# Kernel optimization log

Hardware: AMD Instinct MI355X
Metric: run time of the kernel (lower is better)

## Reference

```python
import jax, jax.numpy as jnp
import numpy as np

DIM = 384
B = 256
EPS = 1e-5


def _conv_replicate(x, W, pad):
    # x: [B,C,H,W], W: [O,I,kh,kw]; replicate (edge) padding then VALID conv
    x = jnp.pad(x, ((0, 0), (0, 0), (pad, pad), (pad, pad)), mode='edge')
    return jax.lax.conv_general_dilated(
        x, W, window_strides=(1, 1), padding='VALID',
        dimension_numbers=('NCHW', 'OIHW', 'NCHW'))


def _bn(x, g, b, m, v):
    scale = (g / jnp.sqrt(v + EPS))[None, :, None, None]
    return (x - m[None, :, None, None]) * scale + b[None, :, None, None]


def _clip_features(target, bbox):
    # target: [B, 576, C] -> vectorized per-sample crop + nearest resize to 12x12
    bb = bbox * 24.0
    x, y, w, h = bb[:, 0], bb[:, 1], bb[:, 2], bb[:, 3]
    l = (w + h) / 2
    l = jnp.sqrt((w + l) * (h + l))
    x_min = jnp.clip(jnp.ceil(x - l / 2), 0, 23).astype(jnp.int32)
    y_min = jnp.clip(jnp.ceil(y - l / 2), 0, 23).astype(jnp.int32)
    x_max = jnp.clip(jnp.trunc(x + l / 2), 0, 23).astype(jnp.int32)
    y_max = jnp.clip(jnp.trunc(y + l / 2), 0, 23).astype(jnp.int32)
    i12 = jnp.arange(12, dtype=jnp.int32)
    # nearest-neighbor source index: crop_start + floor(i * crop_size / 12)
    rows = y_min[:, None] + (i12[None, :] * (y_max - y_min)[:, None]) // 12  # [B,12]
    cols = x_min[:, None] + (i12[None, :] * (x_max - x_min)[:, None]) // 12  # [B,12]
    rows = jnp.clip(rows, 0, 23)
    cols = jnp.clip(cols, 0, 23)
    Bn, N, C = target.shape
    tflat = jnp.transpose(target, (0, 2, 1))  # [B, C, 576] (row-major 24x24)
    idx = rows[:, :, None] * 24 + cols[:, None, :]  # [B,12,12]
    idx = jnp.broadcast_to(idx.reshape(Bn, 1, 144), (Bn, C, 144))
    out = jnp.take_along_axis(tflat, idx, axis=2)  # [B, C, 144]
    return out.reshape(Bn, C, 12, 12)


def setup_inputs() -> dict:
    key = jax.random.key(0)
    ks = jax.random.split(key, 8)
    temp = jax.random.normal(ks[0], (B, 144, DIM), dtype=jnp.float32)
    target = jax.random.normal(ks[1], (B, 576, DIM), dtype=jnp.float32)
    u = jax.random.uniform(ks[2], (B, 4), dtype=jnp.float32)
    # centers in [0.3,0.7], sizes in [0.25,0.45] -> always a valid non-empty crop
    bbox = jnp.concatenate([0.3 + 0.4 * u[:, :2], 0.25 + 0.2 * u[:, 2:]], axis=1)
    W1 = jax.random.normal(ks[3], (DIM, DIM, 5, 5), dtype=jnp.float32) * 0.02
    W2 = jax.random.normal(ks[4], (DIM, DIM, 3, 3), dtype=jnp.float32) * 0.05
    g1 = jnp.ones((DIM,), jnp.float32)
    b1 = jnp.zeros((DIM,), jnp.float32)
    m1 = jax.random.normal(ks[5], (DIM,), dtype=jnp.float32) * 0.1
    v1 = jnp.ones((DIM,), jnp.float32)
    g2 = jnp.ones((DIM,), jnp.float32)
    b2 = jnp.zeros((DIM,), jnp.float32)
    m2 = jax.random.normal(ks[6], (DIM,), dtype=jnp.float32) * 0.1
    v2 = jnp.ones((DIM,), jnp.float32)
    return dict(temp=temp, target=target, bbox=bbox, W1=W1, g1=g1, b1=b1,
                m1=m1, v1=v1, W2=W2, g2=g2, b2=b2, m2=m2, v2=v2)


def reference(temp, target, bbox, W1, g1, b1, m1, v1, W2, g2, b2, m2, v2):
    ta = _clip_features(target, bbox)  # [B, C, 12, 12]
    h1 = jax.nn.leaky_relu(_bn(_conv_replicate(ta, W1, 2), g1, b1, m1, v1), 0.01)
    h2 = jax.nn.leaky_relu(_bn(_conv_replicate(h1, W2, 1), g2, b2, m2, v2), 0.01)
    Bn, N, C = temp.shape
    t = jnp.transpose(temp, (0, 2, 1)).reshape(Bn, C, 12, 12)
    out = (t + h2).reshape(Bn, C, 144)
    return jnp.transpose(out, (0, 2, 1))  # [B, 144, C]
```

## Files before the change

kernel.cpp:

```cpp
#include <hip/hip_runtime.h>
#include <math.h>

#define NBATCH 256
#define CDIM   384

typedef __attribute__((ext_vector_type(4))) float  f32x4;
typedef __attribute__((ext_vector_type(8))) __bf16 bf16x8;
typedef __attribute__((ext_vector_type(4))) __bf16 bf16x4;

__device__ __forceinline__ void load16(const void* g, void* l) {
    __builtin_amdgcn_global_load_lds(
        (const __attribute__((address_space(1))) void*)g,
        (__attribute__((address_space(3))) void*)l, 16, 0, 0);
}

__global__ __launch_bounds__(256) void gather_bf16(
    const float* __restrict__ target,
    const float* __restrict__ bbox,
    __bf16* __restrict__ ta)
{
    const int b = blockIdx.x, t = threadIdx.x;
    __shared__ int pos[144];

    if (t < 144) {
        const float bx0 = bbox[b * 4 + 0] * 24.f;
        const float by0 = bbox[b * 4 + 1] * 24.f;
        const float bw  = bbox[b * 4 + 2] * 24.f;
        const float bh  = bbox[b * 4 + 3] * 24.f;
        const float l0 = (bw + bh) * 0.5f;
        const float l  = sqrtf((bw + l0) * (bh + l0));
        const int xmin = (int)fminf(fmaxf(ceilf (bx0 - l * 0.5f), 0.f), 23.f);
        const int ymin = (int)fminf(fmaxf(ceilf (by0 - l * 0.5f), 0.f), 23.f);
        const int xmax = (int)fminf(fmaxf(truncf(bx0 + l * 0.5f), 0.f), 23.f);
        const int ymax = (int)fminf(fmaxf(truncf(by0 + l * 0.5f), 0.f), 23.f);
        const int i = t / 12, j = t % 12;
        int r = ymin + (i * (ymax - ymin)) / 12;
        int c = xmin + (j * (xmax - xmin)) / 12;
        r = min(max(r, 0), 23);
        c = min(max(c, 0), 23);
        pos[t] = r * 24 + c;
    }
    __syncthreads();

    const float* tb  = target + (size_t)b * 576 * 384;
    __bf16*      tab = ta     + (size_t)b * 144 * 384;
    for (int idx = t; idx < 144 * 96; idx += 256) {
        const int p = idx / 96, c4 = idx - p * 96;
        const float4 v = *(const float4*)&tb[(size_t)pos[p] * 384 + c4 * 4];
        bf16x4 o = { (__bf16)v.x, (__bf16)v.y, (__bf16)v.z, (__bf16)v.w };
        *(bf16x4*)&tab[(size_t)p * 384 + c4 * 4] = o;
    }
}

template <int TAPS>
__global__ __launch_bounds__(256) void prep_w(
    const float* __restrict__ W, __bf16* __restrict__ Wt)
{
    const int K = TAPS * 384;
    __shared__ float ws[TAPS * 384];
    const int oc = blockIdx.x;
    const float* src = W + (size_t)oc * K;
    for (int i = threadIdx.x; i < K; i += 256) ws[i] = src[i];
    __syncthreads();
    __bf16* dst = Wt + (size_t)oc * K;
    for (int i = threadIdx.x; i < K; i += 256) {
        const int tap = i / 384;
        const int ic  = i - tap * 384;
        dst[i] = (__bf16)ws[ic * TAPS + tap];
    }
}

template <int TAPS, int KW, int PAD, bool RESID>
__global__ __launch_bounds__(256, 3) void conv_mfma(
    const __bf16* __restrict__ A,
    const __bf16* __restrict__ Wt,
    const float* __restrict__ gg, const float* __restrict__ bb,
    const float* __restrict__ mm, const float* __restrict__ vv,
    const float* __restrict__ temp,
    void* __restrict__ outp)
{
    const int K  = TAPS * 384;
    const int IT = TAPS * 12;
    const int m0 = blockIdx.x * 128;
    const int n0 = blockIdx.y * 128;
    const int t  = threadIdx.x;
    const int lane  = t & 63, w = t >> 6;
    const int wm    = (w & 1) * 64, wn = (w >> 1) * 64;
    const int col16 = lane & 15,  quad = lane >> 4;

    __shared__ __bf16 As0[128 * 32], As1[128 * 32];
    __shared__ __bf16 Bs0[128 * 32], Bs1[128 * 32];

    const int r0   = t >> 2, slot = t & 3;
    const int kg   = slot ^ ((r0 >> 1) & 3);
    const int mrow0 = m0 + r0, mrow1 = m0 + r0 + 64;
    const int b0 = mrow0 / 144, p0 = mrow0 - b0 * 144;
    const int b1 = mrow1 / 144, p1 = mrow1 - b1 * 144;
    const int y0 = p0 / 12, x0 = p0 - y0 * 12;
    const int y1 = p1 / 12, x1 = p1 - y1 * 12;
    const __bf16* Ab0 = A + (size_t)b0 * 144 * 384 + kg * 8;
    const __bf16* Ab1 = A + (size_t)b1 * 144 * 384 + kg * 8;

    int offA[4], offB[4];
#pragma unroll
    for (int mi = 0; mi < 4; ++mi) {
        const int r = wm + mi * 16 + col16;
        offA[mi] = r * 32 + (quad ^ ((r >> 1) & 3)) * 8;
    }
#pragma unroll
    for (int ni = 0; ni < 4; ++ni) {
        const int r = wn + ni * 16 + col16;
        offB[ni] = r * 32 + (quad ^ ((r >> 1) & 3)) * 8;
    }

    f32x4 acc[4][4];
#pragma unroll
    for (int mi = 0; mi < 4; ++mi)
#pragma unroll
        for (int ni = 0; ni < 4; ++ni)
            acc[mi][ni] = (f32x4){0.f, 0.f, 0.f, 0.f};

    int jn = 0, tapn = 0;
    const __bf16* aT0;
    const __bf16* aT1;
    {
        const int sy0 = min(max(y0 - PAD, 0), 11), sx0 = min(max(x0 - PAD, 0), 11);
        const int sy1 = min(max(y1 - PAD, 0), 11), sx1 = min(max(x1 - PAD, 0), 11);
        aT0 = Ab0 + (size_t)(sy0 * 12 + sx0) * 384;
        aT1 = Ab1 + (size_t)(sy1 * 12 + sx1) * 384;
    }
    const __bf16* bT0 = Wt + (size_t)(n0 + r0)      * K + kg * 8;
    const __bf16* bT1 = Wt + (size_t)(n0 + r0 + 64) * K + kg * 8;

    auto issue = [&](__bf16* SA, __bf16* SB) {
        load16(aT0 + jn * 32, &SA[t * 8]);
        load16(aT1 + jn * 32, &SA[(t + 256) * 8]);
        load16(bT0 + jn * 32, &SB[t * 8]);
        load16(bT1 + jn * 32, &SB[(t + 256) * 8]);
    };
    auto advance = [&]() {
        if (++jn == 12) {
            jn = 0;
            ++tapn;
            if (tapn < TAPS) {
                const int ky = tapn / KW - PAD, kx = tapn % KW - PAD;
                const int sy0 = min(max(y0 + ky, 0), 11), sx0 = min(max(x0 + kx, 0), 11);
                const int sy1 = min(max(y1 + ky, 0), 11), sx1 = min(max(x1 + kx, 0), 11);
                aT0 = Ab0 + (size_t)(sy0 * 12 + sx0) * 384;
                aT1 = Ab1 + (size_t)(sy1 * 12 + sx1) * 384;
                bT0 += 384;
                bT1 += 384;
            }
        }
    };
    auto mfma_step = [&](const __bf16* SA, const __bf16* SB, bool do_issue,
                         __bf16* NA, __bf16* NB_) {
        __syncthreads();
        bf16x8 av[4], bv[4];
#pragma unroll
        for (int mi = 0; mi < 4; ++mi) av[mi] = *(const bf16x8*)&SA[offA[mi]];
#pragma unroll
        for (int ni = 0; ni < 4; ++ni) bv[ni] = *(const bf16x8*)&SB[offB[ni]];
        if (do_issue) issue(NA, NB_);
#pragma unroll
        for (int mi = 0; mi < 4; ++mi)
#pragma unroll
            for (int ni = 0; ni < 4; ++ni)
                acc[mi][ni] = __builtin_amdgcn_mfma_f32_16x16x32_bf16(
                    av[mi], bv[ni], acc[mi][ni], 0, 0, 0);
    };

    issue(As0, Bs0);

    for (int it2 = 0; it2 < IT; it2 += 2) {
        advance();
        mfma_step(As0, Bs0, true, As1, Bs1);
        advance();
        mfma_step(As1, Bs1, it2 + 2 < IT, As0, Bs0);
    }

#pragma unroll
    for (int ni = 0; ni < 4; ++ni) {
        const int gn = n0 + wn + ni * 16 + col16;
        const float scale = gg[gn] * rsqrtf(vv[gn] + 1e-5f);
        const float shift = bb[gn] - mm[gn] * scale;
        if (!RESID) {
            __bf16* h1 = (__bf16*)outp;
#pragma unroll
            for (int mi = 0; mi < 4; ++mi) {
                const int gm = m0 + wm + mi * 16 + quad * 4;
#pragma unroll
                for (int r = 0; r < 4; ++r) {
                    float v = acc[mi][ni][r] * scale + shift;
                    v = (v >= 0.f) ? v : 0.01f * v;
                    h1[(size_t)(gm + r) * 384 + gn] = (__bf16)v;
                }
            }
        } else {
            float* outF = (float*)outp;
#pragma unroll
            for (int mi = 0; mi < 4; ++mi) {
                const int gm = m0 + wm + mi * 16 + quad * 4;
#pragma unroll
                for (int r = 0; r < 4; ++r) {
                    float v = acc[mi][ni][r] * scale + shift;
                    v = (v >= 0.f) ? v : 0.01f * v;
                    outF[(size_t)(gm + r) * 384 + gn] =
                        temp[(size_t)(gm + r) * 384 + gn] + v;
                }
            }
        }
    }
}

extern "C" void kernel_launch(void* const* d_in, const int* in_sizes, int n_in,
                              void* d_out, int out_size, void* d_ws, size_t ws_size,
                              hipStream_t stream) {
    const float* temp   = (const float*)d_in[0];
    const float* target = (const float*)d_in[1];
    const float* bbox   = (const float*)d_in[2];
    const float* W1     = (const float*)d_in[3];
    const float* g1     = (const float*)d_in[4];
    const float* b1     = (const float*)d_in[5];
    const float* m1     = (const float*)d_in[6];
    const float* v1     = (const float*)d_in[7];
    const float* W2     = (const float*)d_in[8];
    const float* g2     = (const float*)d_in[9];
    const float* b2     = (const float*)d_in[10];
    const float* m2     = (const float*)d_in[11];
    const float* v2     = (const float*)d_in[12];
    float* out = (float*)d_out;

    __bf16* ta  = (__bf16*)d_ws;
    __bf16* h1  = ta  + (size_t)NBATCH * 144 * CDIM;
    __bf16* Wt1 = h1  + (size_t)NBATCH * 144 * CDIM;
    __bf16* Wt2 = Wt1 + (size_t)CDIM * 25 * CDIM;

    prep_w<25><<<dim3(CDIM), dim3(256), 0, stream>>>(W1, Wt1);
    prep_w<9><<<dim3(CDIM), dim3(256), 0, stream>>>(W2, Wt2);
    gather_bf16<<<dim3(NBATCH), dim3(256), 0, stream>>>(target, bbox, ta);

    conv_mfma<25, 5, 2, false><<<dim3(288, 3), dim3(256), 0, stream>>>(
        ta, Wt1, g1, b1, m1, v1, nullptr, (void*)h1);
    conv_mfma<9, 3, 1, true><<<dim3(288, 3), dim3(256), 0, stream>>>(
        h1, Wt2, g2, b2, m2, v2, temp, (void*)out);
}
```

Before: 901.9 us.

## Triple-buffer LDS tiles with explicit vmcnt waits in conv MFMA loop

Replaces the double-buffered K loop with a three-stage ring of LDS buffers, keeping two tile loads in flight. Each step waits with a manual s_waitcnt vmcnt(4) plus a raw s_barrier instead of __syncthreads, and raises wave priority around the MFMA block with s_setprio. The goal is to hide global-to-LDS load latency behind compute. In exchange LDS use grows from 32KB to 48KB per block, which may limit the requested 3 blocks per CU, and the hand-written wait counts must stay in step with the four loads issued per stage.

```diff
diff --git a/kernel.cpp b/kernel.cpp
--- a/kernel.cpp
+++ b/kernel.cpp
@@ -88,8 +88,8 @@
     const int wm    = (w & 1) * 64, wn = (w >> 1) * 64;
     const int col16 = lane & 15,  quad = lane >> 4;
 
-    __shared__ __bf16 As0[128 * 32], As1[128 * 32];
-    __shared__ __bf16 Bs0[128 * 32], Bs1[128 * 32];
+    __shared__ __bf16 As0[128 * 32], As1[128 * 32], As2[128 * 32];
+    __shared__ __bf16 Bs0[128 * 32], Bs1[128 * 32], Bs2[128 * 32];
 
     const int r0   = t >> 2, slot = t & 3;
     const int kg   = slot ^ ((r0 >> 1) & 3);
@@ -120,7 +120,7 @@
         for (int ni = 0; ni < 4; ++ni)
             acc[mi][ni] = (f32x4){0.f, 0.f, 0.f, 0.f};
 
-    int jn = 0, tapn = 0;
+    int jn = 0, tapn = 0, next = 0;
     const __bf16* aT0;
     const __bf16* aT1;
     {
@@ -153,30 +153,35 @@
             }
         }
     };
-    auto mfma_step = [&](const __bf16* SA, const __bf16* SB, bool do_issue,
-                         __bf16* NA, __bf16* NB_) {
-        __syncthreads();
+    auto step = [&](const __bf16* SA, const __bf16* SB,
+                    __bf16* NA, __bf16* NB_, bool last) {
+        if (last) asm volatile("s_waitcnt vmcnt(0)" ::: "memory");
+        else      asm volatile("s_waitcnt vmcnt(4)" ::: "memory");
+        __builtin_amdgcn_s_barrier();
+        __builtin_amdgcn_sched_barrier(0);
+        if (next < IT) { issue(NA, NB_); advance(); ++next; }
         bf16x8 av[4], bv[4];
 #pragma unroll
         for (int mi = 0; mi < 4; ++mi) av[mi] = *(const bf16x8*)&SA[offA[mi]];
 #pragma unroll
         for (int ni = 0; ni < 4; ++ni) bv[ni] = *(const bf16x8*)&SB[offB[ni]];
-        if (do_issue) issue(NA, NB_);
+        __builtin_amdgcn_s_setprio(1);
 #pragma unroll
         for (int mi = 0; mi < 4; ++mi)
 #pragma unroll
             for (int ni = 0; ni < 4; ++ni)
                 acc[mi][ni] = __builtin_amdgcn_mfma_f32_16x16x32_bf16(
                     av[mi], bv[ni], acc[mi][ni], 0, 0, 0);
+        __builtin_amdgcn_s_setprio(0);
     };
 
-    issue(As0, Bs0);
-
-    for (int it2 = 0; it2 < IT; it2 += 2) {
-        advance();
-        mfma_step(As0, Bs0, true, As1, Bs1);
-        advance();
-        mfma_step(As1, Bs1, it2 + 2 < IT, As0, Bs0);
+    issue(As0, Bs0); advance(); ++next;
+    issue(As1, Bs1); advance(); ++next;
+
+    for (int it3 = 0; it3 < IT; it3 += 3) {
+        step(As0, Bs0, As2, Bs2, it3 + 1 == IT);
+        step(As1, Bs1, As0, Bs0, it3 + 2 == IT);
+        step(As2, Bs2, As1, Bs1, it3 + 3 == IT);
     }
 
 #pragma unroll
```

Result: faster. 835.4 us (-7.4%).
